# Performance work log

Hardware: AMD Instinct MI355X
Metric: run time of the kernel (lower is better)

The kernel has to match this reference:

```python
import jax, jax.numpy as jnp
import numpy as np

LAYER_START = 4
WIN = 2          # context_window_size (over the LAYER axis)
NORM_EPS = 1e-12 # F.normalize eps
COS_EPS = 1e-8   # cosine_similarity eps


def _alpha_for_k(sf, k, nlay):
    """Alignment/novelty weights for layer k. sf: [B, Ttok, Lay, H].
    Mirrors torch: left = tf[k-w:k] (empty when k<w due to python slicing),
    right = tf[k+1:k+w+1], self row last; QR of window_matrix.T."""
    left = list(range(k - WIN, k)) if k >= WIN else []
    right = list(range(k + 1, min(k + WIN + 1, nlay)))
    rows = left + right + [k]
    m = len(rows)  # 3..5
    W = sf[:, :, jnp.array(rows), :]          # [B,T,m,H]
    A = jnp.swapaxes(W, -1, -2)               # [B,T,H,m]  (window_matrix.T)
    _, R = jnp.linalg.qr(A)                   # reduced: R [B,T,m,m]
    r = R[..., :, -1]                         # [B,T,m]
    Rsub = R[..., :-1, :-1]                   # [B,T,m-1,m-1]
    coln = Rsub / jnp.maximum(jnp.linalg.norm(Rsub, axis=-2, keepdims=True), NORM_EPS)
    row_mean = jnp.mean(coln, axis=-1)        # mean over columns -> [B,T,m-1]
    align = jnp.sum(row_mean * R[..., :-1, -1], axis=-1) / jnp.linalg.norm(r[..., :-1], axis=-1)
    align = 1.0 / (align * m * 2)
    novelty = jnp.abs(r[..., -1]) / jnp.linalg.norm(r, axis=-1)
    return align, novelty


def wk_forward(all_hidden_states, attention_mask):
    # [NL,B,T,H] -> [B, Lay, T, H] after layer_start slice
    emb = jnp.transpose(all_hidden_states, (1, 0, 2, 3))[:, LAYER_START:, :, :]
    B, Lay, T, H = emb.shape
    ntok = T - 1  # attention_mask is all-ones: unmask_num = sum(mask) - 1
    sf = jnp.transpose(emb[:, :, :ntok, :], (0, 2, 1, 3))  # [B,Ttok,Lay,H]
    aligns, novs = [], []
    for k in range(Lay):  # small fixed loop over 9 layers
        a, n = _alpha_for_k(sf, k, Lay)
        aligns.append(a)
        novs.append(n)
    align = jnp.stack(aligns, axis=-1)  # [B,Ttok,Lay]
    nov = jnp.stack(novs, axis=-1)
    align = align / jnp.sum(align, axis=-1, keepdims=True)
    nov = nov / jnp.sum(nov, axis=-1, keepdims=True)
    alpha = align + nov
    alpha = alpha / jnp.sum(alpha, axis=-1, keepdims=True)
    token_emb = jnp.einsum('btl,btlh->bth', alpha, sf)  # unify_token output per token
    # unify_sentence: per-token variance (unbiased) of consecutive-layer cosine sims
    a, b = sf[:, :, 1:, :], sf[:, :, :-1, :]
    num = jnp.sum(a * b, axis=-1)
    den = jnp.maximum(jnp.linalg.norm(a, axis=-1) * jnp.linalg.norm(b, axis=-1), COS_EPS)
    sims = num / den                              # [B,Ttok,Lay-1]
    var_tok = jnp.var(sims, axis=-1, ddof=1)      # torch.var default unbiased
    var_tok = var_tok / jnp.sum(var_tok, axis=-1, keepdims=True)
    return jnp.einsum('bt,bth->bh', var_tok, token_emb)  # [B,H]


def setup_inputs() -> dict:
    key = jax.random.key(0)
    NL, B, T, H = 13, 8, 512, 768
    all_hidden_states = jax.random.normal(key, (NL, B, T, H), dtype=jnp.float32)
    attention_mask = jnp.ones((B, T), dtype=jnp.int32)
    return {"all_hidden_states": all_hidden_states, "attention_mask": attention_mask}


def reference(all_hidden_states, attention_mask):
    return wk_forward(all_hidden_states, attention_mask)
```

## Files before the change

kernel.cpp:

```cpp
#include <hip/hip_runtime.h>
#include <math.h>

#define B_DIM 8
#define T_DIM 512
#define H_DIM 768
#define NTOK 511
#define NLAY 9
#define LAYER_START 4
#define NPAIR 45
#define TCHUNK 128

__device__ float g_part[B_DIM * TCHUNK * H_DIM];
__device__ float g_varp[B_DIM * TCHUNK];

__device__ __forceinline__ int pidx(int lo, int hi) {
  return lo * 9 - lo * (lo - 1) / 2 + (hi - lo);
}

__global__ __launch_bounds__(256, 4) void wk_a(const float* __restrict__ ahs) {
  const int chunk = blockIdx.x;
  const int b = blockIdx.y;
  const int wave = threadIdx.x >> 6;
  const int lane = threadIdx.x & 63;
  const int t_raw = chunk * 4 + wave;
  const bool active = (t_raw < NTOK);
  const int t = active ? t_raw : (NTOK - 1);

  __shared__ float sG[4][48];
  __shared__ float lds_out[4][H_DIM];
  __shared__ float lds_var[4];

  float4 v[NLAY][3];
#pragma unroll
  for (int l = 0; l < NLAY; ++l) {
    const float* base =
        ahs + (((size_t)(l + LAYER_START) * B_DIM + b) * T_DIM + t) * H_DIM;
#pragma unroll
    for (int s = 0; s < 3; ++s) {
      v[l][s] = *reinterpret_cast<const float4*>(base + s * 256 + lane * 4);
    }
  }

  float g[NPAIR];
#pragma unroll
  for (int i = 0; i < NLAY; ++i) {
#pragma unroll
    for (int kk = i; kk < NLAY; ++kk) {
      float s0 = 0.f;
#pragma unroll
      for (int s = 0; s < 3; ++s) {
        s0 += v[i][s].x * v[kk][s].x;
        s0 += v[i][s].y * v[kk][s].y;
        s0 += v[i][s].z * v[kk][s].z;
        s0 += v[i][s].w * v[kk][s].w;
      }
      g[pidx(i, kk)] = s0;
    }
  }

#pragma unroll
  for (int off = 32; off > 0; off >>= 1) {
#pragma unroll
    for (int p = 0; p < NPAIR; ++p) g[p] += __shfl_xor(g[p], off, 64);
  }

  if (lane == 0) {
#pragma unroll
    for (int p = 0; p < NPAIR; ++p) sG[wave][p] = g[p];
  }
  __syncthreads();

  const int k = lane < NLAY ? lane : NLAY - 1;
  const int nl = (k >= 2) ? 2 : 0;
  const int nrr = (NLAY - 1 - k) < 2 ? (NLAY - 1 - k) : 2;
  const int m = nl + nrr + 1;

  auto rowf = [&](int i) -> int {
    return (i < nl) ? (k - 2 + i) : ((i < nl + nrr) ? (k + 1 + i - nl) : k);
  };
  auto GK = [&](int i, int j) -> float {
    int a = rowf(i), c = rowf(j);
    int lo = a < c ? a : c;
    int hi = a < c ? c : a;
    return sG[wave][lo * 9 - lo * (lo - 1) / 2 + (hi - lo)];
  };

  float R[5][5];
#pragma unroll
  for (int j = 0; j < 5; ++j)
#pragma unroll
    for (int i = 0; i < 5; ++i) R[i][j] = 0.f;

#pragma unroll
  for (int j = 0; j < 5; ++j) {
    if (j < m) {
#pragma unroll
      for (int i = 0; i < 5; ++i) {
        if (i < j) {
          float s = GK(i, j);
#pragma unroll
          for (int p = 0; p < 4; ++p)
            if (p < i) s -= R[p][i] * R[p][j];
          R[i][j] = s / R[i][i];
        }
      }
      float sjj = GK(j, j);
#pragma unroll
      for (int p = 0; p < 4; ++p)
        if (p < j) sjj -= R[p][j] * R[p][j];
      R[j][j] = sqrtf(fmaxf(sjj, 0.f));
    }
  }

  float r[5];
#pragma unroll
  for (int i = 0; i < 5; ++i)
    r[i] = (m == 3) ? R[i][2] : ((m == 4) ? R[i][3] : R[i][4]);

  float rowmean[4] = {0.f, 0.f, 0.f, 0.f};
#pragma unroll
  for (int j = 0; j < 4; ++j) {
    if (j < m - 1) {
      float cn = 0.f;
#pragma unroll
      for (int i = 0; i < 4; ++i)
        if (i <= j) cn += R[i][j] * R[i][j];
      cn = fmaxf(sqrtf(cn), 1e-12f);
      float inv = 1.f / cn;
#pragma unroll
      for (int i = 0; i < 4; ++i)
        if (i < m - 1) rowmean[i] += R[i][j] * inv;
    }
  }

  const float inv_m1 = 1.f / (float)(m - 1);
  float dotv = 0.f, nrm2 = 0.f;
#pragma unroll
  for (int i = 0; i < 4; ++i) {
    if (i < m - 1) {
      dotv += (rowmean[i] * inv_m1) * r[i];
      nrm2 += r[i] * r[i];
    }
  }
  float align_raw = dotv / sqrtf(nrm2);
  float align_v = 1.f / (align_raw * (float)m * 2.f);
  float rlast = (m == 3) ? r[2] : ((m == 4) ? r[3] : r[4]);
  float nov_v = fabsf(rlast) / sqrtf(nrm2 + rlast * rlast);

  float al[NLAY], nv[NLAY];
  float asum = 0.f, nsum = 0.f;
#pragma unroll
  for (int l = 0; l < NLAY; ++l) {
    al[l] = __shfl(align_v, l, 64);
    nv[l] = __shfl(nov_v, l, 64);
    asum += al[l];
    nsum += nv[l];
  }
  float alpha[NLAY];
  float csum = 0.f;
#pragma unroll
  for (int l = 0; l < NLAY; ++l) {
    alpha[l] = al[l] / asum + nv[l] / nsum;
    csum += alpha[l];
  }
  const float inv_csum = 1.f / csum;

  float sims[NLAY - 1];
  float smean = 0.f;
#pragma unroll
  for (int j = 0; j < NLAY - 1; ++j) {
    float num = sG[wave][pidx(j, j + 1)];
    float den =
        fmaxf(sqrtf(sG[wave][pidx(j, j)]) * sqrtf(sG[wave][pidx(j + 1, j + 1)]),
              1e-8f);
    sims[j] = num / den;
    smean += sims[j];
  }
  smean *= (1.f / 8.f);
  float var = 0.f;
#pragma unroll
  for (int j = 0; j < NLAY - 1; ++j) {
    float d = sims[j] - smean;
    var += d * d;
  }
  var *= (1.f / 7.f);
  if (!active) var = 0.f;

  if (lane == 0) lds_var[wave] = var;

  float c[NLAY];
#pragma unroll
  for (int l = 0; l < NLAY; ++l) c[l] = var * alpha[l] * inv_csum;

#pragma unroll
  for (int s = 0; s < 3; ++s) {
    float4 o;
    o.x = 0.f; o.y = 0.f; o.z = 0.f; o.w = 0.f;
#pragma unroll
    for (int l = 0; l < NLAY; ++l) {
      o.x += c[l] * v[l][s].x;
      o.y += c[l] * v[l][s].y;
      o.z += c[l] * v[l][s].z;
      o.w += c[l] * v[l][s].w;
    }
    *reinterpret_cast<float4*>(&lds_out[wave][s * 256 + lane * 4]) = o;
  }
  __syncthreads();

  float* dst = g_part + ((size_t)(b * TCHUNK + chunk)) * H_DIM;
#pragma unroll
  for (int s = 0; s < 3; ++s) {
    int h = s * 256 + threadIdx.x;
    float sum = lds_out[0][h] + lds_out[1][h] + lds_out[2][h] + lds_out[3][h];
    dst[h] = sum;
  }
  if (threadIdx.x == 0) {
    g_varp[b * TCHUNK + chunk] =
        lds_var[0] + lds_var[1] + lds_var[2] + lds_var[3];
  }
}

__global__ __launch_bounds__(256) void wk_r(float* __restrict__ out) {
  const int b = blockIdx.y;
  const int h = blockIdx.x * 256 + threadIdx.x;

  float acc = 0.f;
#pragma unroll 8
  for (int j = 0; j < TCHUNK; ++j)
    acc += g_part[((size_t)(b * TCHUNK + j)) * H_DIM + h];

  float ssum = 0.f;
#pragma unroll 8
  for (int j = 0; j < TCHUNK; ++j) ssum += g_varp[b * TCHUNK + j];

  out[b * H_DIM + h] = acc / ssum;
}

extern "C" void kernel_launch(void* const* d_in, const int* in_sizes, int n_in,
                              void* d_out, int out_size, void* d_ws, size_t ws_size,
                              hipStream_t stream) {
  const float* ahs = (const float*)d_in[0];
  float* out = (float*)d_out;
  (void)d_ws; (void)ws_size;

  wk_a<<<dim3(TCHUNK, B_DIM), dim3(256), 0, stream>>>(ahs);
  wk_r<<<dim3(3, B_DIM), dim3(256), 0, stream>>>(out);
}
```

Before: 269.5 us.

## Compute only banded Gram entries and re-read hidden states instead of holding them in registers

The Gram accumulation now covers only pairs within distance 4 (35 band entries rather than 45), which is all the windowed QR and the adjacent-layer cosine need. That shrinks shuffle reductions and LDS use. The 27 float4 register copies of the token's layers are gone; each 256-wide slice is streamed in a non-unrolled loop and read again from global memory for the weighted sum. This cuts register pressure to allow more occupancy, at the cost of reading the input twice (the second pass may hit cache).

```diff
diff --git a/kernel.cpp b/kernel.cpp
--- a/kernel.cpp
+++ b/kernel.cpp
@@ -7,15 +7,13 @@
 #define NTOK 511
 #define NLAY 9
 #define LAYER_START 4
-#define NPAIR 45
+#define NBAND 35
 #define TCHUNK 128
 
 __device__ float g_part[B_DIM * TCHUNK * H_DIM];
 __device__ float g_varp[B_DIM * TCHUNK];
 
-__device__ __forceinline__ int pidx(int lo, int hi) {
-  return lo * 9 - lo * (lo - 1) / 2 + (hi - lo);
-}
+#define BOFF(d) ((d)*9 - (d) * ((d)-1) / 2)
 
 __global__ __launch_bounds__(256, 4) void wk_a(const float* __restrict__ ahs) {
   const int chunk = blockIdx.x;
@@ -26,47 +24,44 @@
   const bool active = (t_raw < NTOK);
   const int t = active ? t_raw : (NTOK - 1);
 
-  __shared__ float sG[4][48];
+  __shared__ float sG[4][36];
   __shared__ float lds_out[4][H_DIM];
   __shared__ float lds_var[4];
 
-  float4 v[NLAY][3];
-#pragma unroll
-  for (int l = 0; l < NLAY; ++l) {
-    const float* base =
-        ahs + (((size_t)(l + LAYER_START) * B_DIM + b) * T_DIM + t) * H_DIM;
-#pragma unroll
-    for (int s = 0; s < 3; ++s) {
-      v[l][s] = *reinterpret_cast<const float4*>(base + s * 256 + lane * 4);
-    }
-  }
-
-  float g[NPAIR];
-#pragma unroll
-  for (int i = 0; i < NLAY; ++i) {
-#pragma unroll
-    for (int kk = i; kk < NLAY; ++kk) {
-      float s0 = 0.f;
-#pragma unroll
-      for (int s = 0; s < 3; ++s) {
-        s0 += v[i][s].x * v[kk][s].x;
-        s0 += v[i][s].y * v[kk][s].y;
-        s0 += v[i][s].z * v[kk][s].z;
-        s0 += v[i][s].w * v[kk][s].w;
+  const size_t LSTR = (size_t)B_DIM * T_DIM * H_DIM;
+  const float* lay0 =
+      ahs + (size_t)LAYER_START * LSTR + ((size_t)b * T_DIM + t) * H_DIM;
+
+  float g[NBAND];
+#pragma unroll
+  for (int p = 0; p < NBAND; ++p) g[p] = 0.f;
+
+#pragma unroll 1
+  for (int s = 0; s < 3; ++s) {
+    const float* p0 = lay0 + s * 256 + lane * 4;
+    float4 vs[NLAY];
+#pragma unroll
+    for (int l = 0; l < NLAY; ++l)
+      vs[l] = *reinterpret_cast<const float4*>(p0 + (size_t)l * LSTR);
+#pragma unroll
+    for (int d = 0; d <= 4; ++d) {
+#pragma unroll
+      for (int i = 0; i + d < NLAY; ++i) {
+        const float4 x = vs[i], y = vs[i + d];
+        g[BOFF(d) + i] += x.x * y.x + x.y * y.y + x.z * y.z + x.w * y.w;
       }
-      g[pidx(i, kk)] = s0;
     }
   }
 
 #pragma unroll
   for (int off = 32; off > 0; off >>= 1) {
 #pragma unroll
-    for (int p = 0; p < NPAIR; ++p) g[p] += __shfl_xor(g[p], off, 64);
+    for (int p = 0; p < NBAND; ++p) g[p] += __shfl_xor(g[p], off, 64);
   }
 
   if (lane == 0) {
 #pragma unroll
-    for (int p = 0; p < NPAIR; ++p) sG[wave][p] = g[p];
+    for (int p = 0; p < NBAND; ++p) sG[wave][p] = g[p];
   }
   __syncthreads();
 
@@ -81,8 +76,8 @@
   auto GK = [&](int i, int j) -> float {
     int a = rowf(i), c = rowf(j);
     int lo = a < c ? a : c;
-    int hi = a < c ? c : a;
-    return sG[wave][lo * 9 - lo * (lo - 1) / 2 + (hi - lo)];
+    int d = (a < c ? c : a) - lo;
+    return sG[wave][d * 9 - d * (d - 1) / 2 + lo];
   };
 
   float R[5][5];
@@ -169,10 +164,8 @@
   float smean = 0.f;
 #pragma unroll
   for (int j = 0; j < NLAY - 1; ++j) {
-    float num = sG[wave][pidx(j, j + 1)];
-    float den =
-        fmaxf(sqrtf(sG[wave][pidx(j, j)]) * sqrtf(sG[wave][pidx(j + 1, j + 1)]),
-              1e-8f);
+    float num = sG[wave][BOFF(1) + j];
+    float den = fmaxf(sqrtf(sG[wave][j]) * sqrtf(sG[wave][j + 1]), 1e-8f);
     sims[j] = num / den;
     smean += sims[j];
   }
@@ -192,16 +185,18 @@
 #pragma unroll
   for (int l = 0; l < NLAY; ++l) c[l] = var * alpha[l] * inv_csum;
 
-#pragma unroll
+#pragma unroll 1
   for (int s = 0; s < 3; ++s) {
+    const float* p0 = lay0 + s * 256 + lane * 4;
     float4 o;
     o.x = 0.f; o.y = 0.f; o.z = 0.f; o.w = 0.f;
 #pragma unroll
     for (int l = 0; l < NLAY; ++l) {
-      o.x += c[l] * v[l][s].x;
-      o.y += c[l] * v[l][s].y;
-      o.z += c[l] * v[l][s].z;
-      o.w += c[l] * v[l][s].w;
+      const float4 vv = *reinterpret_cast<const float4*>(p0 + (size_t)l * LSTR);
+      o.x += c[l] * vv.x;
+      o.y += c[l] * vv.y;
+      o.z += c[l] * vv.z;
+      o.w += c[l] * vv.w;
     }
     *reinterpret_cast<float4*>(&lds_out[wave][s * 256 + lane * 4]) = o;
   }
```

After: 241.0 us. -10.6%, faster.
